# Performance work log

Measured on AMD Instinct MI355X. Metric: run time of the kernel, lower is better.

The kernel has to match this reference:

```python
import jax, jax.numpy as jnp
import numpy as np

N, E, F, H, L, G = 100000, 1600000, 32, 128, 4, 64


def gru_cell(m, h, w_ih, b_ih, w_hh, b_hh):
    # torch.nn.GRUCell math; gate order: r, z, n
    gi = m @ w_ih.T + b_ih          # [N, 3H]
    gh = h @ w_hh.T + b_hh          # [N, 3H]
    i_r, i_z, i_n = jnp.split(gi, 3, axis=-1)
    h_r, h_z, h_n = jnp.split(gh, 3, axis=-1)
    r = jax.nn.sigmoid(i_r + h_r)
    z = jax.nn.sigmoid(i_z + h_z)
    n = jnp.tanh(i_n + r * h_n)
    return (1.0 - z) * n + z * h


def setup_inputs() -> dict:
    key = jax.random.key(0)
    ks = jax.random.split(key, 12)
    s = 0.05
    return {
        "x": jax.random.normal(ks[0], (N, F), jnp.float32),
        "edge_index": jax.random.randint(ks[1], (2, E), 0, N, jnp.int64),
        "batch": jnp.sort(jax.random.randint(ks[2], (N,), 0, G, jnp.int64)),
        "num_graphs": G,
        "W0": jax.random.normal(ks[3], (H, F), jnp.float32) * s,
        "conv_w": jax.random.normal(ks[4], (L, H, H), jnp.float32) * s,
        "w_ih": jax.random.normal(ks[5], (3 * H, H), jnp.float32) * s,
        "b_ih": jax.random.normal(ks[6], (3 * H,), jnp.float32) * s,
        "w_hh": jax.random.normal(ks[7], (3 * H, H), jnp.float32) * s,
        "b_hh": jax.random.normal(ks[8], (3 * H,), jnp.float32) * s,
        "lin1_w": jax.random.normal(ks[9], (1, H), jnp.float32) * s,
        "lin1_b": jax.random.normal(ks[10], (1,), jnp.float32) * s,
    }


def reference(x, edge_index, batch, num_graphs, W0, conv_w, w_ih, b_ih, w_hh, b_hh, lin1_w, lin1_b):
    n_nodes = x.shape[0]
    # lin0 (no bias) + sigmoid embedding
    x_embed = jax.nn.sigmoid(x @ W0.T)                     # [N, H]

    src, dst = edge_index[0], edge_index[1]
    h = x_embed
    # GatedGraphConv: per layer, transform -> scatter-add over edges -> GRU update
    for l in range(conv_w.shape[0]):
        m = h @ conv_w[l]                                   # [N, H]
        agg = jax.ops.segment_sum(m[src], dst, num_segments=n_nodes)  # [N, H]
        h = gru_cell(agg, h, w_ih, b_ih, w_hh, b_hh)

    h = jax.nn.relu(h)
    out = h @ lin1_w.T + lin1_b                             # [N, 1]
    uncorrected = out

    # per-graph mean subtraction (scatter_mean + gather), same math as the loop
    sums = jax.ops.segment_sum(out, batch, num_segments=num_graphs)   # [G, 1]
    counts = jax.ops.segment_sum(jnp.ones((n_nodes, 1), out.dtype), batch, num_segments=num_graphs)
    mean_all = sums / jnp.maximum(counts, 1.0)
    corrected = out - mean_all[batch]

    return corrected.squeeze(1), x_embed, uncorrected.squeeze(1)
```

## Files before the change

kernel.cpp:

```cpp
#include <hip/hip_runtime.h>
#include <hip/hip_bf16.h>

#define HDIM 128
#define FDIM 32
#define GGR  64
#define SCAN_CHUNK 2048
#define FILL_CHUNK 1024
#define FILL_WIN 16

typedef __attribute__((ext_vector_type(8))) short bf16x8;
typedef __attribute__((ext_vector_type(4))) float f32x4;

__device__ __forceinline__ float fsig(float x) {
  return __builtin_amdgcn_rcpf(1.f + __expf(-x));
}
__device__ __forceinline__ float ftanh(float x) {
  return 1.f - 2.f * __builtin_amdgcn_rcpf(1.f + __expf(2.f * x));
}

__device__ __forceinline__ bf16x8 pack_bf16x8(float4 a, float4 b) {
  union { bf16x8 v; __hip_bfloat162 h[4]; } u;
  u.h[0] = __float22bfloat162_rn(make_float2(a.x, a.y));
  u.h[1] = __float22bfloat162_rn(make_float2(a.z, a.w));
  u.h[2] = __float22bfloat162_rn(make_float2(b.x, b.y));
  u.h[3] = __float22bfloat162_rn(make_float2(b.z, b.w));
  return u.v;
}

__device__ __forceinline__ int ablk(int kb, int m) {
  return (kb << 6) + (m & 56) + ((m ^ kb) & 7);
}

__device__ __forceinline__ void stage64(const unsigned short* __restrict__ g,
                                        short* __restrict__ s, int n0, int N, int t) {
#pragma unroll
  for (int r = 0; r < 2; ++r) {
    int idx = r * 512 + t;
    int m = idx >> 4, c8 = idx & 15;
    int gn = n0 + m;
    uint4 v = make_uint4(0u, 0u, 0u, 0u);
    if (gn < N) v = *(const uint4*)(g + (size_t)gn * HDIM + c8 * 8);
    *(uint4*)(s + ablk(c8, m) * 8) = v;
  }
}


__global__ __launch_bounds__(256) void k_embed_hist(const float* __restrict__ x,
                                                    const unsigned short* __restrict__ W0b,
                                                    unsigned short* __restrict__ hb,
                                                    float* __restrict__ xemb,
                                                    const unsigned short* __restrict__ convT0,
                                                    unsigned short* __restrict__ m_out,
                                                    int N,
                                                    const int* __restrict__ dst,
                                                    int* __restrict__ deg,
                                                    unsigned short* __restrict__ rank,
                                                    long long E, int histBlocks, int q8) {
  __shared__ short sE[16 * 64 * 8];
  if ((int)blockIdx.x < histBlocks) {
    long long e = (long long)blockIdx.x * 256 + threadIdx.x;
    if (e < E) {
      int old = atomicAdd(&deg[dst[e]], 1);
      rank[e] = (unsigned short)old;
    }
    return;
  }
  int p = blockIdx.x - histBlocks;
  int T = (p & 7) * q8 + (p >> 3);
  int n0 = T * 64;
  if (n0 >= N) return;
  int t = threadIdx.x;
  int w = t >> 6, l = t & 63;
  int lm = l & 15, lq = l >> 4;
  int j0 = w * 32;
  bf16x8 b0 = *(const bf16x8*)(W0b + (size_t)(j0 + lm) * FDIM + lq * 8);
  bf16x8 b1 = *(const bf16x8*)(W0b + (size_t)(j0 + 16 + lm) * FDIM + lq * 8);
  f32x4 acc0[4], acc1[4];
#pragma unroll
  for (int i = 0; i < 4; ++i) { acc0[i] = (f32x4){0.f,0.f,0.f,0.f}; acc1[i] = (f32x4){0.f,0.f,0.f,0.f}; }
#pragma unroll
  for (int tt = 0; tt < 4; ++tt) {
    int rg = n0 + tt * 16 + lm;
    bf16x8 a = (bf16x8){0,0,0,0,0,0,0,0};
    if (rg < N) {
      const float4* xr = (const float4*)x + (size_t)rg * 8 + lq * 2;
      a = pack_bf16x8(xr[0], xr[1]);
    }
    acc0[tt] = __builtin_amdgcn_mfma_f32_16x16x32_bf16(a, b0, acc0[tt], 0, 0, 0);
    acc1[tt] = __builtin_amdgcn_mfma_f32_16x16x32_bf16(a, b1, acc1[tt], 0, 0, 0);
  }
#pragma unroll
  for (int g = 0; g < 2; ++g) {
    int j = j0 + g * 16 + lm;
#pragma unroll
    for (int tt = 0; tt < 4; ++tt)
#pragma unroll
      for (int r = 0; r < 4; ++r) {
        int m = tt * 16 + lq * 4 + r;
        int node = n0 + m;
        float v = g ? acc1[tt][r] : acc0[tt][r];
        float e = fsig(v);
        __hip_bfloat16 eb = __float2bfloat16(e);
        ((__hip_bfloat16*)sE)[ablk(j >> 3, m) * 8 + (j & 7)] = eb;
        if (node < N) {
          size_t off = (size_t)node * HDIM + j;
          xemb[off] = e;
          ((__hip_bfloat16*)hb)[off] = eb;
        }
      }
  }
  __syncthreads();
#pragma unroll
  for (int g = 0; g < 2; ++g) {
    int jg = j0 + g * 16;
    f32x4 macc[4];
#pragma unroll
    for (int i = 0; i < 4; ++i) macc[i] = (f32x4){0.f,0.f,0.f,0.f};
#pragma unroll
    for (int ks = 0; ks < 4; ++ks) {
      bf16x8 b = *(const bf16x8*)(convT0 + (size_t)(jg + lm) * HDIM + ks * 32 + lq * 8);
      int kb = ks * 4 + lq;
#pragma unroll
      for (int tt = 0; tt < 4; ++tt) {
        bf16x8 a = *(const bf16x8*)(sE + ablk(kb, tt * 16 + lm) * 8);
        macc[tt] = __builtin_amdgcn_mfma_f32_16x16x32_bf16(a, b, macc[tt], 0, 0, 0);
      }
    }
    int j = jg + lm;
#pragma unroll
    for (int tt = 0; tt < 4; ++tt)
#pragma unroll
      for (int r = 0; r < 4; ++r) {
        int node = n0 + tt * 16 + lq * 4 + r;
        if (node < N)
          ((__hip_bfloat16*)m_out)[(size_t)node * HDIM + j] = __float2bfloat16(macc[tt][r]);
      }
  }
}

__global__ __launch_bounds__(256) void k_prep_w(const float* __restrict__ w_ih,
                                                const float* __restrict__ w_hh,
                                                const float* __restrict__ conv_w,
                                                const float* __restrict__ W0,
                                                unsigned short* __restrict__ wIb,
                                                unsigned short* __restrict__ wHb,
                                                unsigned short* __restrict__ convTb,
                                                unsigned short* __restrict__ W0b,
                                                int L) {
  int i = blockIdx.x * 256 + threadIdx.x;
  if (i < HDIM * FDIM) ((__hip_bfloat16*)W0b)[i] = __float2bfloat16(W0[i]);
  if (i < 384 * HDIM) {
    ((__hip_bfloat16*)wIb)[i] = __float2bfloat16(w_ih[i]);
    ((__hip_bfloat16*)wHb)[i] = __float2bfloat16(w_hh[i]);
  }
  int total = L * HDIM * HDIM;
  if (i < total) {
    int l = i >> 14, rem = i & 16383, j = rem >> 7, k = rem & 127;
    ((__hip_bfloat16*)convTb)[i] = __float2bfloat16(conv_w[(l << 14) + (k << 7) + j]);
  }
}

__global__ __launch_bounds__(256) void k_block_sum(const int* __restrict__ deg,
                                                   int* __restrict__ bsum, int N) {
  int base = blockIdx.x * SCAN_CHUNK + threadIdx.x * 8;
  int s = 0;
#pragma unroll
  for (int u = 0; u < 8; ++u) { int i = base + u; if (i < N) s += deg[i]; }
#pragma unroll
  for (int o = 32; o; o >>= 1) s += __shfl_down(s, o, 64);
  __shared__ int wsum[4];
  if ((threadIdx.x & 63) == 0) wsum[threadIdx.x >> 6] = s;
  __syncthreads();
  if (threadIdx.x == 0) bsum[blockIdx.x] = wsum[0] + wsum[1] + wsum[2] + wsum[3];
}

__global__ void k_scan_bsums(int* __restrict__ bsum, int nb) {
  if (blockIdx.x == 0 && threadIdx.x == 0) {
    int run = 0;
    for (int i = 0; i < nb; ++i) { int v = bsum[i]; bsum[i] = run; run += v; }
  }
}

__global__ __launch_bounds__(256) void k_scan_chunks(const int* __restrict__ deg,
                                                     const int* __restrict__ bsum,
                                                     int* __restrict__ rowstart,
                                                     int N, int Etot) {
  __shared__ int ts[256];
  int base = blockIdx.x * SCAN_CHUNK + threadIdx.x * 8;
  int loc[8]; int s = 0;
#pragma unroll
  for (int u = 0; u < 8; ++u) {
    int i = base + u; loc[u] = s;
    s += (i < N) ? deg[i] : 0;
  }
  ts[threadIdx.x] = s;
  __syncthreads();
  for (int o = 1; o < 256; o <<= 1) {
    int v = (threadIdx.x >= o) ? ts[threadIdx.x - o] : 0;
    __syncthreads();
    ts[threadIdx.x] += v;
    __syncthreads();
  }
  int texcl = (threadIdx.x ? ts[threadIdx.x - 1] : 0) + bsum[blockIdx.x];
#pragma unroll
  for (int u = 0; u < 8; ++u) {
    int i = base + u;
    if (i < N) rowstart[i] = texcl + loc[u];
  }
  if (blockIdx.x == 0 && threadIdx.x == 0) rowstart[N] = Etot;
}

__global__ __launch_bounds__(256) void k_csr_fill_win(const int* __restrict__ src,
                                                      const int* __restrict__ dst,
                                                      const unsigned short* __restrict__ rank,
                                                      const int* __restrict__ rowstart,
                                                      int* __restrict__ csr,
                                                      long long E, int N) {
  __shared__ int sd[FILL_CHUNK];
  __shared__ int ss[FILL_CHUNK];
  __shared__ unsigned short sr[FILL_CHUNK];
  long long base = (long long)blockIdx.x * FILL_CHUNK;
  int cnt = (int)((E - base < FILL_CHUNK) ? (E - base) : FILL_CHUNK);
  for (int i = threadIdx.x; i < cnt; i += 256) {
    sd[i] = dst[base + i];
    ss[i] = src[base + i];
    sr[i] = rank[base + i];
  }
  __syncthreads();
  int nw = (N + FILL_WIN - 1) / FILL_WIN;
#pragma unroll 1
  for (int w = 0; w < FILL_WIN; ++w) {
    int lo = w * nw, hi = lo + nw;
    for (int i = threadIdx.x; i < cnt; i += 256) {
      int d = sd[i];
      if (d >= lo && d < hi)
        csr[rowstart[d] + sr[i]] = ss[i];
    }
    __syncthreads();
  }
}

__global__ __launch_bounds__(256) void k_gather(const int* __restrict__ csr,
                                                const int* __restrict__ rowstart,
                                                const unsigned short* __restrict__ m,
                                                unsigned short* __restrict__ agg, int N, int q8) {
  int p = blockIdx.x;
  int G = (p & 7) * q8 * 16 + (p >> 3);
  int wv = threadIdx.x >> 6, l = threadIdx.x & 63;
  int n = G * 4 + wv;
  if (n >= N) return;
  int eq = l >> 3;
  int jb = l & 7;
  int beg = rowstart[n], end = rowstart[n + 1];
  float acc[16];
#pragma unroll
  for (int i = 0; i < 16; ++i) acc[i] = 0.f;
  for (int e0 = beg; e0 < end; e0 += 8) {
    int e = e0 + eq;
    uint4 v0 = make_uint4(0u, 0u, 0u, 0u);
    uint4 v1 = make_uint4(0u, 0u, 0u, 0u);
    if (e < end) {
      int s = csr[e];
      const uint4* row = (const uint4*)(m + (size_t)s * HDIM + jb * 16);
      v0 = row[0];
      v1 = row[1];
    }
    acc[0]  += __uint_as_float(v0.x << 16);
    acc[1]  += __uint_as_float(v0.x & 0xffff0000u);
    acc[2]  += __uint_as_float(v0.y << 16);
    acc[3]  += __uint_as_float(v0.y & 0xffff0000u);
    acc[4]  += __uint_as_float(v0.z << 16);
    acc[5]  += __uint_as_float(v0.z & 0xffff0000u);
    acc[6]  += __uint_as_float(v0.w << 16);
    acc[7]  += __uint_as_float(v0.w & 0xffff0000u);
    acc[8]  += __uint_as_float(v1.x << 16);
    acc[9]  += __uint_as_float(v1.x & 0xffff0000u);
    acc[10] += __uint_as_float(v1.y << 16);
    acc[11] += __uint_as_float(v1.y & 0xffff0000u);
    acc[12] += __uint_as_float(v1.z << 16);
    acc[13] += __uint_as_float(v1.z & 0xffff0000u);
    acc[14] += __uint_as_float(v1.w << 16);
    acc[15] += __uint_as_float(v1.w & 0xffff0000u);
  }
#pragma unroll
  for (int i = 0; i < 16; ++i) {
    acc[i] += __shfl_xor(acc[i], 8, 64);
    acc[i] += __shfl_xor(acc[i], 16, 64);
    acc[i] += __shfl_xor(acc[i], 32, 64);
  }
  if (eq == 0) {
    union { uint4 v[2]; __hip_bfloat162 h[8]; } o;
#pragma unroll
    for (int i = 0; i < 8; ++i)
      o.h[i] = __float22bfloat162_rn(make_float2(acc[2 * i], acc[2 * i + 1]));
    uint4* dstp = (uint4*)(agg + (size_t)n * HDIM + jb * 16);
    dstp[0] = o.v[0];
    dstp[1] = o.v[1];
  }
}

__global__ __launch_bounds__(512, 4) void k_gru_mfma(const unsigned short* __restrict__ aggb,
                                                  const unsigned short* __restrict__ hb,
                                                  const unsigned short* __restrict__ wI,
                                                  const unsigned short* __restrict__ wH,
                                                  const float* __restrict__ b_ih,
                                                  const float* __restrict__ b_hh,
                                                  unsigned short* __restrict__ hnewb,
                                                  const unsigned short* __restrict__ wT,
                                                  unsigned short* __restrict__ m_out,
                                                  int N, int q8) {
  __shared__ short sAg[16 * 64 * 8];
  __shared__ short sH[16 * 64 * 8];
  int p = blockIdx.x;
  int T = (p & 7) * q8 + (p >> 3);
  int n0 = T * 64;
  if (n0 >= N) return;
  int t = threadIdx.x;
  stage64(aggb, sAg, n0, N, t);
  stage64(hb, sH, n0, N, t);
  int w = t >> 6, l = t & 63;
  int j0 = w * 16;
  int lm = l & 15, lq = l >> 4;
  int j = j0 + lm;
  float bir = b_ih[j], biz = b_ih[j + 128], bin = b_ih[j + 256];
  float bhr = b_hh[j], bhz = b_hh[j + 128], bhn = b_hh[j + 256];
  __syncthreads();
  f32x4 aR[4], aZ[4], aNi[4], aNh[4];
#pragma unroll
  for (int i = 0; i < 4; ++i) {
    aR[i] = (f32x4){0.f,0.f,0.f,0.f}; aZ[i] = (f32x4){0.f,0.f,0.f,0.f};
    aNi[i] = (f32x4){0.f,0.f,0.f,0.f}; aNh[i] = (f32x4){0.f,0.f,0.f,0.f};
  }
#pragma unroll
  for (int ks = 0; ks < 4; ++ks) {
    size_t rI = (size_t)(j0 + lm) * HDIM + ks * 32 + lq * 8;
    bf16x8 bIr = *(const bf16x8*)(wI + rI);
    bf16x8 bIz = *(const bf16x8*)(wI + rI + 128 * HDIM);
    bf16x8 bIn = *(const bf16x8*)(wI + rI + 256 * HDIM);
    bf16x8 bHr = *(const bf16x8*)(wH + rI);
    bf16x8 bHz = *(const bf16x8*)(wH + rI + 128 * HDIM);
    bf16x8 bHn = *(const bf16x8*)(wH + rI + 256 * HDIM);
    int kb = ks * 4 + lq;
#pragma unroll
    for (int tt = 0; tt < 4; ++tt) {
      bf16x8 a = *(const bf16x8*)(sAg + ablk(kb, tt * 16 + lm) * 8);
      bf16x8 h = *(const bf16x8*)(sH + ablk(kb, tt * 16 + lm) * 8);
      aR[tt] = __builtin_amdgcn_mfma_f32_16x16x32_bf16(a, bIr, aR[tt], 0, 0, 0);
      aR[tt] = __builtin_amdgcn_mfma_f32_16x16x32_bf16(h, bHr, aR[tt], 0, 0, 0);
      aZ[tt] = __builtin_amdgcn_mfma_f32_16x16x32_bf16(a, bIz, aZ[tt], 0, 0, 0);
      aZ[tt] = __builtin_amdgcn_mfma_f32_16x16x32_bf16(h, bHz, aZ[tt], 0, 0, 0);
      aNi[tt] = __builtin_amdgcn_mfma_f32_16x16x32_bf16(a, bIn, aNi[tt], 0, 0, 0);
      aNh[tt] = __builtin_amdgcn_mfma_f32_16x16x32_bf16(h, bHn, aNh[tt], 0, 0, 0);
    }
  }
  __syncthreads();
#pragma unroll
  for (int tt = 0; tt < 4; ++tt)
#pragma unroll
    for (int r = 0; r < 4; ++r) {
      int m = tt * 16 + lq * 4 + r;
      int node = n0 + m;
      float hp = __bfloat162float(((const __hip_bfloat16*)sH)[ablk(j >> 3, m) * 8 + (j & 7)]);
      float rg = fsig(aR[tt][r] + bir + bhr);
      float zg = fsig(aZ[tt][r] + biz + bhz);
      float nv = aNi[tt][r] + bin + rg * (aNh[tt][r] + bhn);
      float th = ftanh(nv);
      float hn = (1.f - zg) * th + zg * hp;
      __hip_bfloat16 hnb = __float2bfloat16(hn);
      ((__hip_bfloat16*)sAg)[ablk(j >> 3, m) * 8 + (j & 7)] = hnb;
      if (node < N)
        ((__hip_bfloat16*)hnewb)[(size_t)node * HDIM + j] = hnb;
    }
  if (wT) {
    __syncthreads();
    f32x4 macc[4];
#pragma unroll
    for (int i = 0; i < 4; ++i) macc[i] = (f32x4){0.f,0.f,0.f,0.f};
#pragma unroll
    for (int ks = 0; ks < 4; ++ks) {
      bf16x8 b = *(const bf16x8*)(wT + (size_t)(j0 + lm) * HDIM + ks * 32 + lq * 8);
      int kb = ks * 4 + lq;
#pragma unroll
      for (int tt = 0; tt < 4; ++tt) {
        bf16x8 a = *(const bf16x8*)(sAg + ablk(kb, tt * 16 + lm) * 8);
        macc[tt] = __builtin_amdgcn_mfma_f32_16x16x32_bf16(a, b, macc[tt], 0, 0, 0);
      }
    }
#pragma unroll
    for (int tt = 0; tt < 4; ++tt)
#pragma unroll
      for (int r = 0; r < 4; ++r) {
        int node = n0 + tt * 16 + lq * 4 + r;
        if (node < N)
          ((__hip_bfloat16*)m_out)[(size_t)node * HDIM + j] = __float2bfloat16(macc[tt][r]);
      }
  }
}

__global__ __launch_bounds__(256) void k_readout(const unsigned short* __restrict__ h,
                                                 const float* __restrict__ w1,
                                                 const float* __restrict__ b1,
                                                 float* __restrict__ out_raw,
                                                 float* __restrict__ uncorrected,
                                                 int N) {
  int wave = threadIdx.x >> 6;
  int lane = threadIdx.x & 63;
  int n = blockIdx.x * 4 + wave;
  if (n >= N) return;
  float h0 = __bfloat162float(((const __hip_bfloat16*)h)[(size_t)n * HDIM + lane]);
  float h1 = __bfloat162float(((const __hip_bfloat16*)h)[(size_t)n * HDIM + 64 + lane]);
  float v = fmaxf(h0, 0.f) * w1[lane] + fmaxf(h1, 0.f) * w1[64 + lane];
#pragma unroll
  for (int o = 32; o > 0; o >>= 1) v += __shfl_down(v, o, 64);
  if (lane == 0) {
    float o = v + b1[0];
    out_raw[n] = o;
    uncorrected[n] = o;
  }
}

__global__ __launch_bounds__(256) void k_graph_reduce(const float* __restrict__ out_raw,
                                                      const int* __restrict__ batch,
                                                      float* __restrict__ gsum,
                                                      float* __restrict__ gcnt,
                                                      int N) {
  __shared__ float ls[GGR], lc[GGR];
  int t = threadIdx.x;
  if (t < GGR) { ls[t] = 0.f; lc[t] = 0.f; }
  __syncthreads();
  for (int n = blockIdx.x * 256 + t; n < N; n += gridDim.x * 256) {
    int g = batch[n];
    atomicAdd(&ls[g], out_raw[n]);
    atomicAdd(&lc[g], 1.f);
  }
  __syncthreads();
  if (t < GGR) {
    unsafeAtomicAdd(&gsum[t], ls[t]);
    unsafeAtomicAdd(&gcnt[t], lc[t]);
  }
}

__global__ __launch_bounds__(256) void k_correct(const float* __restrict__ out_raw,
                                                 const int* __restrict__ batch,
                                                 const float* __restrict__ gsum,
                                                 const float* __restrict__ gcnt,
                                                 float* __restrict__ corrected, int N) {
  int n = blockIdx.x * 256 + threadIdx.x;
  if (n < N) {
    int g = batch[n];
    corrected[n] = out_raw[n] - gsum[g] / fmaxf(gcnt[g], 1.f);
  }
}

extern "C" void kernel_launch(void* const* d_in, const int* in_sizes, int n_in,
                              void* d_out, int out_size, void* d_ws, size_t ws_size,
                              hipStream_t stream) {
  const float* x      = (const float*)d_in[0];
  const int*   ei     = (const int*)d_in[1];
  const int*   batch  = (const int*)d_in[2];
  const float* W0     = (const float*)d_in[4];
  const float* conv_w = (const float*)d_in[5];
  const float* w_ih   = (const float*)d_in[6];
  const float* b_ih   = (const float*)d_in[7];
  const float* w_hh   = (const float*)d_in[8];
  const float* b_hh   = (const float*)d_in[9];
  const float* lin1_w = (const float*)d_in[10];
  const float* lin1_b = (const float*)d_in[11];

  int N = in_sizes[0] / FDIM;
  long long E = in_sizes[1] / 2;
  int L = in_sizes[5] / (HDIM * HDIM);

  const int* src = ei;
  const int* dstv = ei + E;

  float* out_corrected = (float*)d_out;
  float* out_xemb = out_corrected + N;
  float* out_unc  = out_xemb + (size_t)N * HDIM;

  char* p = (char*)d_ws;
  unsigned short* x0 = (unsigned short*)p; p += (size_t)N * HDIM * 2;
  unsigned short* x1 = (unsigned short*)p; p += (size_t)N * HDIM * 2;
  unsigned short* x2 = (unsigned short*)p; p += (size_t)N * HDIM * 2;
  float* out_raw = (float*)p;        p += (size_t)((N + 3) & ~3) * 4;
  float* gsum = (float*)p;           p += GGR * 4;
  float* gcnt = (float*)p;           p += GGR * 4;
  int* deg = (int*)p;                p += (size_t)((N + 3) & ~3) * 4;
  int* rowstart = (int*)p;           p += (size_t)(N + 4) * 4;
  int nb = (N + SCAN_CHUNK - 1) / SCAN_CHUNK;
  int* bsum = (int*)p;               p += (size_t)((nb + 63) & ~63) * 4;
  int* csr = (int*)p;                p += (size_t)E * 4;
  unsigned short* rankb = (unsigned short*)p;  p += (size_t)((E + 3) & ~3) * 2;
  unsigned short* wIb = (unsigned short*)p;    p += 384 * HDIM * 2;
  unsigned short* wHb = (unsigned short*)p;    p += 384 * HDIM * 2;
  unsigned short* convTb = (unsigned short*)p; p += (size_t)L * HDIM * HDIM * 2;
  unsigned short* W0b = (unsigned short*)p;

  int prep_total = (384 * HDIM > L * HDIM * HDIM) ? 384 * HDIM : L * HDIM * HDIM;
  k_prep_w<<<(prep_total + 255) / 256, 256, 0, stream>>>(w_ih, w_hh, conv_w, W0, wIb, wHb, convTb, W0b, L);

  hipMemsetAsync(deg, 0, (size_t)N * sizeof(int), stream);

  int nblk = (N + 63) / 64;
  int TP = (nblk + 7) & ~7;
  int q8 = TP / 8;
  int histBlocks = (int)((E + 255) / 256);
  k_embed_hist<<<histBlocks + TP, 256, 0, stream>>>(x, W0b, x0, out_xemb, convTb, x1, N,
                                                    dstv, deg, rankb, E, histBlocks, q8);

  k_block_sum<<<nb, 256, 0, stream>>>(deg, bsum, N);
  k_scan_bsums<<<1, 64, 0, stream>>>(bsum, nb);
  k_scan_chunks<<<nb, 256, 0, stream>>>(deg, bsum, rowstart, N, (int)E);
  k_csr_fill_win<<<(int)((E + FILL_CHUNK - 1) / FILL_CHUNK), 256, 0, stream>>>(
      src, dstv, rankb, rowstart, csr, E, N);

  unsigned short* Hb = x0;
  unsigned short* Mb = x1;
  for (int l = 0; l < L; ++l) {
    k_gather<<<TP * 16, 256, 0, stream>>>(csr, rowstart, Mb, x2, N, q8);
    const unsigned short* wTn = (l + 1 < L) ? (convTb + (size_t)(l + 1) * HDIM * HDIM) : nullptr;
    k_gru_mfma<<<TP, 512, 0, stream>>>(x2, Hb, wIb, wHb, b_ih, b_hh, Mb, wTn, Hb, N, q8);
    unsigned short* tmp = Hb; Hb = Mb; Mb = tmp;
  }

  hipMemsetAsync(gsum, 0, 2 * GGR * sizeof(float), stream);
  k_readout<<<(N + 3) / 4, 256, 0, stream>>>(Hb, lin1_w, lin1_b, out_raw, out_unc, N);
  k_graph_reduce<<<256, 256, 0, stream>>>(out_raw, batch, gsum, gcnt, N);
  k_correct<<<(N + 255) / 256, 256, 0, stream>>>(out_raw, batch, gsum, gcnt, out_corrected, N);
}
```

Baseline: 740.6 us.

## Co-schedule embedding with CSR fill and fuse readout into last GRU layer

The histogram pass no longer shares a launch with the embedding GEMM. The embedding now runs in the same launch as the CSR fill, with interleaved block indices so the compute-bound and scatter-bound work overlap on the device. The final GRU layer computes the relu plus linear readout directly from registers, using shuffle reduction and shared atomics, so the separate readout kernel and the last hidden-state write are no longer needed. This adds branching inside the GRU kernel and reuses the embedding's shared buffer for the fill staging.

```diff
diff --git a/kernel.cpp b/kernel.cpp
--- a/kernel.cpp
+++ b/kernel.cpp
@@ -44,29 +44,63 @@
   }
 }
 
-
-__global__ __launch_bounds__(256) void k_embed_hist(const float* __restrict__ x,
+__global__ __launch_bounds__(256) void k_hist(const int* __restrict__ dst, int* __restrict__ deg,
+                                              unsigned short* __restrict__ rank,
+                                              long long E) {
+  long long e = (long long)blockIdx.x * 256 + threadIdx.x;
+  if (e < E) {
+    int old = atomicAdd(&deg[dst[e]], 1);
+    rank[e] = (unsigned short)old;
+  }
+}
+
+__global__ __launch_bounds__(256) void k_embed_fill(const float* __restrict__ x,
                                                     const unsigned short* __restrict__ W0b,
                                                     unsigned short* __restrict__ hb,
                                                     float* __restrict__ xemb,
                                                     const unsigned short* __restrict__ convT0,
                                                     unsigned short* __restrict__ m_out,
                                                     int N,
+                                                    const int* __restrict__ src,
                                                     const int* __restrict__ dst,
-                                                    int* __restrict__ deg,
-                                                    unsigned short* __restrict__ rank,
-                                                    long long E, int histBlocks, int q8) {
+                                                    const unsigned short* __restrict__ rank,
+                                                    const int* __restrict__ rowstart,
+                                                    int* __restrict__ csr,
+                                                    long long E, int TP, int FB, int q8) {
   __shared__ short sE[16 * 64 * 8];
-  if ((int)blockIdx.x < histBlocks) {
-    long long e = (long long)blockIdx.x * 256 + threadIdx.x;
-    if (e < E) {
-      int old = atomicAdd(&deg[dst[e]], 1);
-      rank[e] = (unsigned short)old;
+  int p = blockIdx.x;
+  int M2 = ((TP < FB) ? TP : FB) * 2;
+  bool isFill; int idx;
+  if (p < M2) { isFill = (p & 1); idx = p >> 1; }
+  else { idx = p - (M2 >> 1); isFill = (FB > TP); }
+
+  if (isFill) {
+    int* sd = (int*)sE;
+    int* ss = sd + FILL_CHUNK;
+    unsigned short* sr = (unsigned short*)(ss + FILL_CHUNK);
+    long long base = (long long)idx * FILL_CHUNK;
+    int cnt = (int)((E - base < FILL_CHUNK) ? (E - base) : FILL_CHUNK);
+    for (int i = threadIdx.x; i < cnt; i += 256) {
+      sd[i] = dst[base + i];
+      ss[i] = src[base + i];
+      sr[i] = rank[base + i];
+    }
+    __syncthreads();
+    int nw = (N + FILL_WIN - 1) / FILL_WIN;
+#pragma unroll 1
+    for (int w = 0; w < FILL_WIN; ++w) {
+      int lo = w * nw, hi = lo + nw;
+      for (int i = threadIdx.x; i < cnt; i += 256) {
+        int d = sd[i];
+        if (d >= lo && d < hi)
+          csr[rowstart[d] + sr[i]] = ss[i];
+      }
+      __syncthreads();
     }
     return;
   }
-  int p = blockIdx.x - histBlocks;
-  int T = (p & 7) * q8 + (p >> 3);
+
+  int T = (idx & 7) * q8 + (idx >> 3);
   int n0 = T * 64;
   if (n0 >= N) return;
   int t = threadIdx.x;
@@ -208,36 +242,6 @@
     if (i < N) rowstart[i] = texcl + loc[u];
   }
   if (blockIdx.x == 0 && threadIdx.x == 0) rowstart[N] = Etot;
-}
-
-__global__ __launch_bounds__(256) void k_csr_fill_win(const int* __restrict__ src,
-                                                      const int* __restrict__ dst,
-                                                      const unsigned short* __restrict__ rank,
-                                                      const int* __restrict__ rowstart,
-                                                      int* __restrict__ csr,
-                                                      long long E, int N) {
-  __shared__ int sd[FILL_CHUNK];
-  __shared__ int ss[FILL_CHUNK];
-  __shared__ unsigned short sr[FILL_CHUNK];
-  long long base = (long long)blockIdx.x * FILL_CHUNK;
-  int cnt = (int)((E - base < FILL_CHUNK) ? (E - base) : FILL_CHUNK);
-  for (int i = threadIdx.x; i < cnt; i += 256) {
-    sd[i] = dst[base + i];
-    ss[i] = src[base + i];
-    sr[i] = rank[base + i];
-  }
-  __syncthreads();
-  int nw = (N + FILL_WIN - 1) / FILL_WIN;
-#pragma unroll 1
-  for (int w = 0; w < FILL_WIN; ++w) {
-    int lo = w * nw, hi = lo + nw;
-    for (int i = threadIdx.x; i < cnt; i += 256) {
-      int d = sd[i];
-      if (d >= lo && d < hi)
-        csr[rowstart[d] + sr[i]] = ss[i];
-    }
-    __syncthreads();
-  }
 }
 
 __global__ __launch_bounds__(256) void k_gather(const int* __restrict__ csr,
@@ -308,9 +312,14 @@
                                                   unsigned short* __restrict__ hnewb,
                                                   const unsigned short* __restrict__ wT,
                                                   unsigned short* __restrict__ m_out,
+                                                  const float* __restrict__ w1,
+                                                  const float* __restrict__ b1,
+                                                  float* __restrict__ out_raw,
+                                                  float* __restrict__ out_unc,
                                                   int N, int q8) {
   __shared__ short sAg[16 * 64 * 8];
   __shared__ short sH[16 * 64 * 8];
+  __shared__ float sOut[64];
   int p = blockIdx.x;
   int T = (p & 7) * q8 + (p >> 3);
   int n0 = T * 64;
@@ -318,12 +327,15 @@
   int t = threadIdx.x;
   stage64(aggb, sAg, n0, N, t);
   stage64(hb, sH, n0, N, t);
+  if (!wT && t < 64) sOut[t] = 0.f;
   int w = t >> 6, l = t & 63;
   int j0 = w * 16;
   int lm = l & 15, lq = l >> 4;
   int j = j0 + lm;
   float bir = b_ih[j], biz = b_ih[j + 128], bin = b_ih[j + 256];
   float bhr = b_hh[j], bhz = b_hh[j + 128], bhn = b_hh[j + 256];
+  float w1j = 0.f;
+  if (!wT) w1j = w1[j];
   __syncthreads();
   f32x4 aR[4], aZ[4], aNi[4], aNh[4];
 #pragma unroll
@@ -366,10 +378,19 @@
       float nv = aNi[tt][r] + bin + rg * (aNh[tt][r] + bhn);
       float th = ftanh(nv);
       float hn = (1.f - zg) * th + zg * hp;
-      __hip_bfloat16 hnb = __float2bfloat16(hn);
-      ((__hip_bfloat16*)sAg)[ablk(j >> 3, m) * 8 + (j & 7)] = hnb;
-      if (node < N)
-        ((__hip_bfloat16*)hnewb)[(size_t)node * HDIM + j] = hnb;
+      if (wT) {
+        __hip_bfloat16 hnb = __float2bfloat16(hn);
+        ((__hip_bfloat16*)sAg)[ablk(j >> 3, m) * 8 + (j & 7)] = hnb;
+        if (node < N)
+          ((__hip_bfloat16*)hnewb)[(size_t)node * HDIM + j] = hnb;
+      } else {
+        float prt = (node < N) ? fmaxf(hn, 0.f) * w1j : 0.f;
+        prt += __shfl_xor(prt, 1, 64);
+        prt += __shfl_xor(prt, 2, 64);
+        prt += __shfl_xor(prt, 4, 64);
+        prt += __shfl_xor(prt, 8, 64);
+        if (lm == 0) atomicAdd(&sOut[m], prt);
+      }
     }
   if (wT) {
     __syncthreads();
@@ -394,28 +415,16 @@
         if (node < N)
           ((__hip_bfloat16*)m_out)[(size_t)node * HDIM + j] = __float2bfloat16(macc[tt][r]);
       }
-  }
-}
-
-__global__ __launch_bounds__(256) void k_readout(const unsigned short* __restrict__ h,
-                                                 const float* __restrict__ w1,
-                                                 const float* __restrict__ b1,
-                                                 float* __restrict__ out_raw,
-                                                 float* __restrict__ uncorrected,
-                                                 int N) {
-  int wave = threadIdx.x >> 6;
-  int lane = threadIdx.x & 63;
-  int n = blockIdx.x * 4 + wave;
-  if (n >= N) return;
-  float h0 = __bfloat162float(((const __hip_bfloat16*)h)[(size_t)n * HDIM + lane]);
-  float h1 = __bfloat162float(((const __hip_bfloat16*)h)[(size_t)n * HDIM + 64 + lane]);
-  float v = fmaxf(h0, 0.f) * w1[lane] + fmaxf(h1, 0.f) * w1[64 + lane];
-#pragma unroll
-  for (int o = 32; o > 0; o >>= 1) v += __shfl_down(v, o, 64);
-  if (lane == 0) {
-    float o = v + b1[0];
-    out_raw[n] = o;
-    uncorrected[n] = o;
+  } else {
+    __syncthreads();
+    if (t < 64) {
+      int node = n0 + t;
+      if (node < N) {
+        float o = sOut[t] + b1[0];
+        out_raw[node] = o;
+        out_unc[node] = o;
+      }
+    }
   }
 }
 
@@ -500,31 +509,32 @@
   k_prep_w<<<(prep_total + 255) / 256, 256, 0, stream>>>(w_ih, w_hh, conv_w, W0, wIb, wHb, convTb, W0b, L);
 
   hipMemsetAsync(deg, 0, (size_t)N * sizeof(int), stream);
+  hipMemsetAsync(gsum, 0, 2 * GGR * sizeof(float), stream);
 
   int nblk = (N + 63) / 64;
   int TP = (nblk + 7) & ~7;
   int q8 = TP / 8;
   int histBlocks = (int)((E + 255) / 256);
-  k_embed_hist<<<histBlocks + TP, 256, 0, stream>>>(x, W0b, x0, out_xemb, convTb, x1, N,
-                                                    dstv, deg, rankb, E, histBlocks, q8);
-
+  int FB = (int)((E + FILL_CHUNK - 1) / FILL_CHUNK);
+
+  k_hist<<<histBlocks, 256, 0, stream>>>(dstv, deg, rankb, E);
   k_block_sum<<<nb, 256, 0, stream>>>(deg, bsum, N);
   k_scan_bsums<<<1, 64, 0, stream>>>(bsum, nb);
   k_scan_chunks<<<nb, 256, 0, stream>>>(deg, bsum, rowstart, N, (int)E);
-  k_csr_fill_win<<<(int)((E + FILL_CHUNK - 1) / FILL_CHUNK), 256, 0, stream>>>(
-      src, dstv, rankb, rowstart, csr, E, N);
+
+  k_embed_fill<<<TP + FB, 256, 0, stream>>>(x, W0b, x0, out_xemb, convTb, x1, N,
+                                            src, dstv, rankb, rowstart, csr, E, TP, FB, q8);
 
   unsigned short* Hb = x0;
   unsigned short* Mb = x1;
   for (int l = 0; l < L; ++l) {
     k_gather<<<TP * 16, 256, 0, stream>>>(csr, rowstart, Mb, x2, N, q8);
     const unsigned short* wTn = (l + 1 < L) ? (convTb + (size_t)(l + 1) * HDIM * HDIM) : nullptr;
-    k_gru_mfma<<<TP, 512, 0, stream>>>(x2, Hb, wIb, wHb, b_ih, b_hh, Mb, wTn, Hb, N, q8);
+    k_gru_mfma<<<TP, 512, 0, stream>>>(x2, Hb, wIb, wHb, b_ih, b_hh, Mb, wTn, Hb,
+                                       lin1_w, lin1_b, out_raw, out_unc, N, q8);
     unsigned short* tmp = Hb; Hb = Mb; Mb = tmp;
   }
 
-  hipMemsetAsync(gsum, 0, 2 * GGR * sizeof(float), stream);
-  k_readout<<<(N + 3) / 4, 256, 0, stream>>>(Hb, lin1_w, lin1_b, out_raw, out_unc, N);
   k_graph_reduce<<<256, 256, 0, stream>>>(out_raw, batch, gsum, gcnt, N);
   k_correct<<<(N + 255) / 256, 256, 0, stream>>>(out_raw, batch, gsum, gcnt, out_corrected, N);
 }
```

Measured after the change: 780.2 us. 5.3% more time.
